# Kernel optimization log

Hardware: AMD Instinct MI355X
Metric: run time of the kernel (lower is better)

The kernel has to match this reference:

```python
import jax, jax.numpy as jnp
import numpy as np

N_EMBD = 1024
HEAD_SIZE = 64

def setup_inputs() -> dict:
    key = jax.random.key(0)
    kx, kk, kq, kv = jax.random.split(key, 4)
    x = jax.random.normal(kx, (8, 2048, N_EMBD), dtype=jnp.float32)
    scale = 1.0 / np.sqrt(N_EMBD)
    # nn.Linear weights are [out, in]; kaiming-uniform-ish init
    Wk = jax.random.uniform(kk, (HEAD_SIZE, N_EMBD), dtype=jnp.float32, minval=-scale, maxval=scale)
    Wq = jax.random.uniform(kq, (HEAD_SIZE, N_EMBD), dtype=jnp.float32, minval=-scale, maxval=scale)
    Wv = jax.random.uniform(kv, (HEAD_SIZE, N_EMBD), dtype=jnp.float32, minval=-scale, maxval=scale)
    return {"x": x, "Wk": Wk, "Wq": Wq, "Wv": Wv}

def reference(x, Wk, Wq, Wv):
    # x: [B, T, E]; W*: [H, E] (torch Linear layout)
    k = jnp.einsum('bte,he->bth', x, Wk)
    q = jnp.einsum('bte,he->bth', x, Wq)
    v = jnp.einsum('bte,he->bth', x, Wv)
    inv_sqrt_h = 1.0 / np.sqrt(HEAD_SIZE)
    wei = jnp.einsum('bth,bsh->bts', q, k) * inv_sqrt_h  # [B, T, T]
    wei = jax.nn.softmax(wei, axis=-1)
    out = jnp.einsum('bts,bsh->bth', wei, v)  # [B, T, H]
    return out
```

## Files before the change

### kernel.cpp

```cpp
#include <hip/hip_runtime.h>
#include <cstdint>

#define NB 8
#define TS 2048
#define NE 1024
#define HD 64
#define MTOT (NB*TS)

typedef float     f4  __attribute__((ext_vector_type(4)));
typedef short     s8v __attribute__((ext_vector_type(8)));
typedef short     s4v __attribute__((ext_vector_type(4)));
typedef int       i4v __attribute__((ext_vector_type(4)));
typedef _Float16  h8  __attribute__((ext_vector_type(8)));

__device__ __forceinline__ short f2bf(float f) {
  union { float f; uint32_t u; } x; x.f = f;
  return (short)((x.u + 0x7FFFu + ((x.u >> 16) & 1u)) >> 16);
}

__device__ __forceinline__ int pack2(float lo, float hi) {
  union { float f; uint32_t u; } a, b; a.f = lo; b.f = hi;
  return (int)__builtin_amdgcn_perm(b.u + 0x8000u, a.u + 0x8000u, 0x07060302u);
}

__device__ __forceinline__ void gl2lds(const void* gptr, void* lptr) {
  auto g = (const __attribute__((address_space(1))) uint32_t*)gptr;
  auto l = (__attribute__((address_space(3))) uint32_t*)lptr;
  __builtin_amdgcn_global_load_lds(g, l, 16, 0, 0);
}

template <int N>
__device__ __forceinline__ void wait_barrier() {
  asm volatile("s_waitcnt vmcnt(%0) lgkmcnt(0)" :: "n"(N) : "memory");
  __builtin_amdgcn_s_barrier();
}

template <int N>
__device__ __forceinline__ void wave_wait() {
  asm volatile("s_waitcnt vmcnt(%0)" :: "n"(N) : "memory");
}

__global__ __launch_bounds__(256) void wconv_kernel(
    const float* __restrict__ Wk, const float* __restrict__ Wq, const float* __restrict__ Wv,
    short* __restrict__ wb)
{
  const int idx = (blockIdx.x * 256 + threadIdx.x) * 4;
  const int p = idx >> 16;
  const int off = idx & 65535;
  const float* W = (p == 0) ? Wq : (p == 1) ? Wk : Wv;
  const float s = (p == 0) ? 0.18033688011112042f : 1.0f;
  const float4 v = *(const float4*)&W[off];
  s4v h; h[0] = f2bf(v.x*s); h[1] = f2bf(v.y*s); h[2] = f2bf(v.z*s); h[3] = f2bf(v.w*s);
  *(s4v*)&wb[idx] = h;
}

__global__ __launch_bounds__(256) void proj_kernel(
    const float* __restrict__ x, const short* __restrict__ wb,
    short* __restrict__ qo, short* __restrict__ ko, _Float16* __restrict__ vo)
{
  __shared__ float Xs[4][32][64];
  __shared__ short Ws[2][192][64];
  const int tid = threadIdx.x;
  const int wv = tid >> 6, lane = tid & 63, n = lane & 15, quad = lane >> 4;
  const int mg = wv & 1, cg = wv >> 1;
  const int r0 = blockIdx.x * 32;
  const int xrow = lane >> 4, xslot = lane & 15;
  const int wrow = lane >> 3, wslot = lane & 7;

  auto dmaX = [&](int c, int buf) {
#pragma unroll
    for (int u = 0; u < 2; ++u) {
      const int R0 = (wv * 2 + u) * 4;
      const int row = R0 + xrow;
      const int gs = (xslot + row) & 15;
      gl2lds(&x[(size_t)(r0 + row) * NE + c * 64 + gs * 4], &Xs[buf][R0][0]);
    }
  };
  auto dmaW = [&](int c, int buf) {
#pragma unroll
    for (int u = 0; u < 6; ++u) {
      const int C0 = (wv * 6 + u) * 8;
      const int col = C0 + wrow;
      const int gs = (wslot + col) & 7;
      gl2lds(&wb[(size_t)col * NE + c * 64 + gs * 8], &Ws[buf][C0][0]);
    }
  };

  const f4 fz = {0.f, 0.f, 0.f, 0.f};
  f4 acc[6] = {fz, fz, fz, fz, fz, fz};

  auto compute = [&](int bw, int bx) {
    s8v a[2];
    const int row = mg * 16 + n;
#pragma unroll
    for (int kc = 0; kc < 2; ++kc) {
      const int u0 = kc * 8 + quad * 2;
      const float* pr = &Xs[bx][row][0];
      const f4 f0 = *(const f4*)(pr + (((u0    ) - row) & 15) * 4);
      const f4 f1 = *(const f4*)(pr + (((u0 + 1) - row) & 15) * 4);
      i4v ai;
      ai[0] = pack2(f0[0], f0[1]); ai[1] = pack2(f0[2], f0[3]);
      ai[2] = pack2(f1[0], f1[1]); ai[3] = pack2(f1[2], f1[3]);
      a[kc] = __builtin_bit_cast(s8v, ai);
    }
#pragma unroll
    for (int nf = 0; nf < 6; ++nf) {
      const int col = cg * 96 + nf * 16 + n;
      const s8v b0 = *(const s8v*)&Ws[bw][col][(((0 + quad) - col) & 7) * 8];
      const s8v b1 = *(const s8v*)&Ws[bw][col][(((4 + quad) - col) & 7) * 8];
      acc[nf] = __builtin_amdgcn_mfma_f32_16x16x32_bf16(a[0], b0, acc[nf], 0, 0, 0);
      acc[nf] = __builtin_amdgcn_mfma_f32_16x16x32_bf16(a[1], b1, acc[nf], 0, 0, 0);
    }
  };

  dmaW(0, 0); dmaX(0, 0); dmaX(1, 1); dmaX(2, 2);
  wait_barrier<4>();

  for (int t = 0; t < 16; ++t) {
    if (t <= 14) dmaW(t + 1, (t + 1) & 1);
    if (t <= 12) dmaX(t + 3, (t + 3) & 3);
    compute(t & 1, t & 3);
    if (t <= 12)      wait_barrier<2>();
    else if (t <= 14) wait_barrier<0>();
  }

#pragma unroll
  for (int nf = 0; nf < 6; ++nf) {
    const int gc = cg * 96 + nf * 16;
    const int p = gc >> 6;
    const int rcol = (gc & 63) + n;
#pragma unroll
    for (int i = 0; i < 4; ++i) {
      const int R = r0 + mg * 16 + quad * 4 + i;
      const float av = acc[nf][i];
      if (p == 0)      qo[(size_t)R * HD + rcol] = f2bf(av);
      else if (p == 1) ko[(size_t)R * HD + rcol] = f2bf(av);
      else {
        const int t2 = R & (TS - 1), b = t2 & 31;
        const int pos = (t2 & ~31) | (((b >> 2) & 3) << 3) | (((b >> 4) & 1) << 2) | (b & 3);
        vo[(size_t)(R >> 11) * HD * TS + (size_t)rcol * TS + pos] = (_Float16)av;
      }
    }
  }
}

__global__ __launch_bounds__(256) void attn_kernel(
    const short* __restrict__ q, const short* __restrict__ k,
    const _Float16* __restrict__ vT, float* __restrict__ out)
{
  __shared__ __align__(16) char smem[65536];
  const int tid = threadIdx.x;
  const int wv = tid >> 6, lane = tid & 63, n = lane & 15, quad = lane >> 4;
  const int kq = wv;
  const int batch = blockIdx.x & 7;
  const int qgb = blockIdx.x >> 3;
  const int m0 = batch * TS + qgb * 32;
  const short*    kb = k  + (size_t)batch * TS * HD;
  const _Float16* vb = vT + (size_t)batch * HD * TS;
  const int krow = lane >> 3, kslot = lane & 7;
  const int vrow = lane >> 2, vslot = lane & 3;
  const f4 fz = {0.f, 0.f, 0.f, 0.f};

  auto kbuf = [&](int buf) { return (short*)   (smem +         (kq * 2 + buf) * 4096); };
  auto vbuf = [&](int buf) { return (_Float16*)(smem + 32768 + (kq * 2 + buf) * 4096); };

  auto dmaKV = [&](int tt, int buf) {
    const int c = kq * 16 + tt;
#pragma unroll
    for (int u = 0; u < 4; ++u) {
      const int K0 = u * 8;
      const int key = K0 + krow;
      const int gs = (kslot + key) & 7;
      gl2lds(&kb[(size_t)(c * 32 + key) * HD + gs * 8], kbuf(buf) + K0 * 64);
    }
#pragma unroll
    for (int u = 0; u < 4; ++u) {
      const int D0 = u * 16;
      const int d = D0 + vrow;
      const int gs = (vslot + d) & 3;
      gl2lds(&vb[(size_t)d * TS + c * 32 + gs * 8], vbuf(buf) + D0 * 32);
    }
  };

  s8v qf[2][2];
#pragma unroll
  for (int qh = 0; qh < 2; ++qh)
#pragma unroll
    for (int kc = 0; kc < 2; ++kc)
      qf[qh][kc] = *(const s8v*)&q[(size_t)(m0 + qh * 16 + n) * HD + kc * 32 + quad * 8];

  f4 o[2][4] = {{fz, fz, fz, fz}, {fz, fz, fz, fz}};
  f4 lD[2] = {fz, fz};
  h8 ones;
#pragma unroll
  for (int j = 0; j < 8; ++j) ones[j] = (_Float16)1.0f;

  dmaKV(0, 0); dmaKV(1, 1);
  wave_wait<8>();

  for (int t = 0; t < 16; ++t) {
    const int buf = t & 1;

    if (t >= 1 && t <= 14) dmaKV(t + 1, (t + 1) & 1);

    const short*    ks = kbuf(buf);
    const _Float16* vs = vbuf(buf);

    f4 st[2][2];
#pragma unroll
    for (int f = 0; f < 2; ++f) {
      const int key = f * 16 + n;
      const s8v k0 = *(const s8v*)&ks[key * 64 + (((0 + quad) - key) & 7) * 8];
      const s8v k1 = *(const s8v*)&ks[key * 64 + (((4 + quad) - key) & 7) * 8];
#pragma unroll
      for (int qh = 0; qh < 2; ++qh) {
        st[qh][f] = __builtin_amdgcn_mfma_f32_16x16x32_bf16(k0, qf[qh][0], fz, 0, 0, 0);
        st[qh][f] = __builtin_amdgcn_mfma_f32_16x16x32_bf16(k1, qf[qh][1], st[qh][f], 0, 0, 0);
      }
    }

    h8 pa[2];
#pragma unroll
    for (int qh = 0; qh < 2; ++qh)
#pragma unroll
      for (int f = 0; f < 2; ++f)
#pragma unroll
        for (int i = 0; i < 4; ++i)
          pa[qh][f * 4 + i] = (_Float16)__builtin_amdgcn_exp2f(st[qh][f][i]);

#pragma unroll
    for (int qh = 0; qh < 2; ++qh)
      lD[qh] = __builtin_amdgcn_mfma_f32_16x16x32_f16(pa[qh], ones, lD[qh], 0, 0, 0);
#pragma unroll
    for (int g = 0; g < 4; ++g) {
      const int d = g * 16 + n;
      const h8 vf = *(const h8*)&vs[d * 32 + ((quad - d) & 3) * 8];
#pragma unroll
      for (int qh = 0; qh < 2; ++qh)
        o[qh][g] = __builtin_amdgcn_mfma_f32_16x16x32_f16(pa[qh], vf, o[qh][g], 0, 0, 0);
    }

    if (t <= 14) wave_wait<0>();
  }

  __syncthreads();

  float* o_c = (float*)smem;
  float* l_c = (float*)(smem + 34816);
  if (n == 0)
#pragma unroll
    for (int qh = 0; qh < 2; ++qh)
#pragma unroll
      for (int i = 0; i < 4; ++i)
        l_c[kq * 32 + qh * 16 + quad * 4 + i] = lD[qh][i];
#pragma unroll
  for (int qh = 0; qh < 2; ++qh)
#pragma unroll
    for (int g = 0; g < 4; ++g)
#pragma unroll
      for (int i = 0; i < 4; ++i)
        o_c[kq * 2176 + (qh * 16 + quad * 4 + i) * 68 + g * 16 + n] = o[qh][g][i];
  __syncthreads();

#pragma unroll
  for (int rep = 0; rep < 2; ++rep) {
    const int idx = tid + rep * 256;
    const int qr = idx >> 4, d4 = (idx & 15) * 4;
    float L = 0.f;
    f4 r = fz;
#pragma unroll
    for (int c2 = 0; c2 < 4; ++c2) {
      L += l_c[c2 * 32 + qr];
      r += *(const f4*)&o_c[c2 * 2176 + qr * 68 + d4];
    }
    const float inv = 1.0f / L;
    r[0] *= inv; r[1] *= inv; r[2] *= inv; r[3] *= inv;
    *(f4*)&out[(size_t)(m0 + qr) * HD + d4] = r;
  }
}

extern "C" void kernel_launch(void* const* d_in, const int* in_sizes, int n_in,
                              void* d_out, int out_size, void* d_ws, size_t ws_size,
                              hipStream_t stream) {
  const float* x  = (const float*)d_in[0];
  const float* Wk = (const float*)d_in[1];
  const float* Wq = (const float*)d_in[2];
  const float* Wv = (const float*)d_in[3];
  float* out = (float*)d_out;

  short* qb = (short*)d_ws;
  short* kb = qb + (size_t)MTOT * HD;
  _Float16* vb = (_Float16*)(kb + (size_t)MTOT * HD);
  short* wb = (short*)(vb + (size_t)NB * HD * TS);

  wconv_kernel<<<192, 256, 0, stream>>>(Wk, Wq, Wv, wb);
  proj_kernel<<<MTOT / 32, 256, 0, stream>>>(x, wb, qb, kb, vb);
  attn_kernel<<<MTOT / 32, 256, 0, stream>>>(qb, kb, vb, out);
}
```

Measured before the change: 131.5 us.

## Process 64 queries per attention block with 8 waves splitting the key range

The attention kernel now runs 512-thread blocks that each handle 64 query rows instead of 32. Each of the 8 waves covers a 256-key slice instead of 512 keys, so every K/V tile staged into LDS is reused across four 16-row query groups rather than two. This halves K/V global and LDS traffic per query and interleaves the QK MFMAs with the exp per query group. In exchange it raises register pressure, grows LDS use to about 138 KB (only one block fits per CU), and makes the final cross-wave reduction of partial outputs and row sums 8-way instead of 4-way.

```diff
diff --git a/kernel.cpp b/kernel.cpp
--- a/kernel.cpp
+++ b/kernel.cpp
@@ -144,28 +144,27 @@
   }
 }
 
-__global__ __launch_bounds__(256) void attn_kernel(
+__global__ __launch_bounds__(512, 2) void attn_kernel(
     const short* __restrict__ q, const short* __restrict__ k,
     const _Float16* __restrict__ vT, float* __restrict__ out)
 {
-  __shared__ __align__(16) char smem[65536];
+  __shared__ __align__(16) char smem[141312];
   const int tid = threadIdx.x;
   const int wv = tid >> 6, lane = tid & 63, n = lane & 15, quad = lane >> 4;
-  const int kq = wv;
   const int batch = blockIdx.x & 7;
   const int qgb = blockIdx.x >> 3;
-  const int m0 = batch * TS + qgb * 32;
+  const int m0 = batch * TS + qgb * 64;
   const short*    kb = k  + (size_t)batch * TS * HD;
   const _Float16* vb = vT + (size_t)batch * HD * TS;
   const int krow = lane >> 3, kslot = lane & 7;
   const int vrow = lane >> 2, vslot = lane & 3;
   const f4 fz = {0.f, 0.f, 0.f, 0.f};
 
-  auto kbuf = [&](int buf) { return (short*)   (smem +         (kq * 2 + buf) * 4096); };
-  auto vbuf = [&](int buf) { return (_Float16*)(smem + 32768 + (kq * 2 + buf) * 4096); };
+  auto kbuf = [&](int buf) { return (short*)   (smem +         (wv * 2 + buf) * 4096); };
+  auto vbuf = [&](int buf) { return (_Float16*)(smem + 65536 + (wv * 2 + buf) * 4096); };
 
   auto dmaKV = [&](int tt, int buf) {
-    const int c = kq * 16 + tt;
+    const int c = wv * 8 + tt;
 #pragma unroll
     for (int u = 0; u < 4; ++u) {
       const int K0 = u * 8;
@@ -182,15 +181,15 @@
     }
   };
 
-  s8v qf[2][2];
-#pragma unroll
-  for (int qh = 0; qh < 2; ++qh)
+  s8v qf[4][2];
+#pragma unroll
+  for (int qh = 0; qh < 4; ++qh)
 #pragma unroll
     for (int kc = 0; kc < 2; ++kc)
       qf[qh][kc] = *(const s8v*)&q[(size_t)(m0 + qh * 16 + n) * HD + kc * 32 + quad * 8];
 
-  f4 o[2][4] = {{fz, fz, fz, fz}, {fz, fz, fz, fz}};
-  f4 lD[2] = {fz, fz};
+  f4 o[4][4] = {{fz, fz, fz, fz}, {fz, fz, fz, fz}, {fz, fz, fz, fz}, {fz, fz, fz, fz}};
+  f4 lD[4] = {fz, fz, fz, fz};
   h8 ones;
 #pragma unroll
   for (int j = 0; j < 8; ++j) ones[j] = (_Float16)1.0f;
@@ -198,80 +197,80 @@
   dmaKV(0, 0); dmaKV(1, 1);
   wave_wait<8>();
 
-  for (int t = 0; t < 16; ++t) {
+  for (int t = 0; t < 8; ++t) {
     const int buf = t & 1;
 
-    if (t >= 1 && t <= 14) dmaKV(t + 1, (t + 1) & 1);
+    if (t >= 1 && t <= 6) dmaKV(t + 1, (t + 1) & 1);
 
     const short*    ks = kbuf(buf);
     const _Float16* vs = vbuf(buf);
 
-    f4 st[2][2];
+    s8v kf[2][2];
 #pragma unroll
     for (int f = 0; f < 2; ++f) {
       const int key = f * 16 + n;
-      const s8v k0 = *(const s8v*)&ks[key * 64 + (((0 + quad) - key) & 7) * 8];
-      const s8v k1 = *(const s8v*)&ks[key * 64 + (((4 + quad) - key) & 7) * 8];
-#pragma unroll
-      for (int qh = 0; qh < 2; ++qh) {
-        st[qh][f] = __builtin_amdgcn_mfma_f32_16x16x32_bf16(k0, qf[qh][0], fz, 0, 0, 0);
-        st[qh][f] = __builtin_amdgcn_mfma_f32_16x16x32_bf16(k1, qf[qh][1], st[qh][f], 0, 0, 0);
+      kf[f][0] = *(const s8v*)&ks[key * 64 + (((0 + quad) - key) & 7) * 8];
+      kf[f][1] = *(const s8v*)&ks[key * 64 + (((4 + quad) - key) & 7) * 8];
+    }
+
+    h8 pa[4];
+#pragma unroll
+    for (int qh = 0; qh < 4; ++qh) {
+      f4 s0 = __builtin_amdgcn_mfma_f32_16x16x32_bf16(kf[0][0], qf[qh][0], fz, 0, 0, 0);
+      s0     = __builtin_amdgcn_mfma_f32_16x16x32_bf16(kf[0][1], qf[qh][1], s0, 0, 0, 0);
+      f4 s1 = __builtin_amdgcn_mfma_f32_16x16x32_bf16(kf[1][0], qf[qh][0], fz, 0, 0, 0);
+      s1     = __builtin_amdgcn_mfma_f32_16x16x32_bf16(kf[1][1], qf[qh][1], s1, 0, 0, 0);
+#pragma unroll
+      for (int i = 0; i < 4; ++i) {
+        pa[qh][i]     = (_Float16)__builtin_amdgcn_exp2f(s0[i]);
+        pa[qh][4 + i] = (_Float16)__builtin_amdgcn_exp2f(s1[i]);
       }
     }
 
-    h8 pa[2];
-#pragma unroll
-    for (int qh = 0; qh < 2; ++qh)
-#pragma unroll
-      for (int f = 0; f < 2; ++f)
-#pragma unroll
-        for (int i = 0; i < 4; ++i)
-          pa[qh][f * 4 + i] = (_Float16)__builtin_amdgcn_exp2f(st[qh][f][i]);
-
-#pragma unroll
-    for (int qh = 0; qh < 2; ++qh)
+#pragma unroll
+    for (int qh = 0; qh < 4; ++qh)
       lD[qh] = __builtin_amdgcn_mfma_f32_16x16x32_f16(pa[qh], ones, lD[qh], 0, 0, 0);
 #pragma unroll
     for (int g = 0; g < 4; ++g) {
       const int d = g * 16 + n;
       const h8 vf = *(const h8*)&vs[d * 32 + ((quad - d) & 3) * 8];
 #pragma unroll
-      for (int qh = 0; qh < 2; ++qh)
+      for (int qh = 0; qh < 4; ++qh)
         o[qh][g] = __builtin_amdgcn_mfma_f32_16x16x32_f16(pa[qh], vf, o[qh][g], 0, 0, 0);
     }
 
-    if (t <= 14) wave_wait<0>();
+    if (t <= 6) wave_wait<0>();
   }
 
   __syncthreads();
 
   float* o_c = (float*)smem;
-  float* l_c = (float*)(smem + 34816);
+  float* l_c = (float*)(smem + 139264);
   if (n == 0)
 #pragma unroll
-    for (int qh = 0; qh < 2; ++qh)
+    for (int qh = 0; qh < 4; ++qh)
 #pragma unroll
       for (int i = 0; i < 4; ++i)
-        l_c[kq * 32 + qh * 16 + quad * 4 + i] = lD[qh][i];
-#pragma unroll
-  for (int qh = 0; qh < 2; ++qh)
+        l_c[wv * 64 + qh * 16 + quad * 4 + i] = lD[qh][i];
+#pragma unroll
+  for (int qh = 0; qh < 4; ++qh)
 #pragma unroll
     for (int g = 0; g < 4; ++g)
 #pragma unroll
       for (int i = 0; i < 4; ++i)
-        o_c[kq * 2176 + (qh * 16 + quad * 4 + i) * 68 + g * 16 + n] = o[qh][g][i];
+        o_c[wv * 4352 + (qh * 16 + quad * 4 + i) * 68 + g * 16 + n] = o[qh][g][i];
   __syncthreads();
 
 #pragma unroll
   for (int rep = 0; rep < 2; ++rep) {
-    const int idx = tid + rep * 256;
+    const int idx = tid + rep * 512;
     const int qr = idx >> 4, d4 = (idx & 15) * 4;
     float L = 0.f;
     f4 r = fz;
 #pragma unroll
-    for (int c2 = 0; c2 < 4; ++c2) {
-      L += l_c[c2 * 32 + qr];
-      r += *(const f4*)&o_c[c2 * 2176 + qr * 68 + d4];
+    for (int c2 = 0; c2 < 8; ++c2) {
+      L += l_c[c2 * 64 + qr];
+      r += *(const f4*)&o_c[c2 * 4352 + qr * 68 + d4];
     }
     const float inv = 1.0f / L;
     r[0] *= inv; r[1] *= inv; r[2] *= inv; r[3] *= inv;
@@ -295,5 +294,5 @@
 
   wconv_kernel<<<192, 256, 0, stream>>>(Wk, Wq, Wv, wb);
   proj_kernel<<<MTOT / 32, 256, 0, stream>>>(x, wb, qb, kb, vb);
-  attn_kernel<<<MTOT / 32, 256, 0, stream>>>(qb, kb, vb, out);
-}
+  attn_kernel<<<MTOT / 64, 512, 0, stream>>>(qb, kb, vb, out);
+}
```

Result: no change. 129.0 us (-1.9%).
